# Performance work log

Measured on AMD Instinct MI355X. Metric: run time of the kernel, lower is better.

## Reference

```python
import jax, jax.numpy as jnp
import numpy as np


def setup_inputs() -> dict:
    key = jax.random.key(0)
    M, N = 2048, 16384
    x = jax.random.normal(key, (M, N), dtype=jnp.float32)
    # expk per DREAMPlace get_expk: exp(-j*pi*n/(2N)) stored as [N, 2] = (cos, -sin)
    ang = jnp.arange(N, dtype=jnp.float32) * np.float32(np.pi / (2.0 * N))
    expk = jnp.stack([jnp.cos(ang), -jnp.sin(ang)], axis=-1)
    return {"x": x, "expk": expk}


def reference(x, expk):
    """IDXCT: y_k = Re{ sum_{n=0}^{N-1} x_n * exp(j*pi/(2N) * n * (2k+1)) }.

    O(N log N) via the FFT trick:
      y_k = Re{ sum_n [x_n * exp(j*pi*n/(2N))] * exp(j*2*pi*n*k/(2N)) }
          = 2N * Re{ IFFT_{2N}(zero-padded v)[k] },  v_n = x_n * conj(expk_n)
    """
    N = x.shape[-1]
    # expk encodes exp(-j*pi*n/(2N)); we need its conjugate exp(+j*pi*n/(2N))
    v = x * (expk[..., 0] - 1j * expk[..., 1])  # complex64, [M, N]
    V = jnp.fft.ifft(v, n=2 * N, axis=-1)       # zero-padded to 2N
    y = (2 * N) * jnp.real(V[..., :N])
    return y.astype(x.dtype)
```

## Files before the change

### kernel.cpp

```cpp
#include <hip/hip_runtime.h>

#define PI_F 3.14159265358979323846f

constexpr int N_COLS   = 16384;
constexpr int HALF     = 8192;
constexpr int NTHREADS = 1024;

__device__ __forceinline__ int sw(int a) {
    return a ^ ((a >> 5) & 31) ^ ((a >> 10) & 31);
}

__global__ __launch_bounds__(NTHREADS)
void idxct_kernel(const float* __restrict__ x,
                  const float* __restrict__ expk,
                  float* __restrict__ y)
{
    __shared__ float sre[HALF];
    __shared__ float sim[HALF];

    const int row = blockIdx.x;
    const float* __restrict__ xr = x + (size_t)row * N_COLS;
    float* __restrict__ yr       = y + (size_t)row * N_COLS;
    const int t = threadIdx.x;
    const float x0 = xr[0];
    const float2* __restrict__ ek2 = (const float2*)expk;

    #pragma unroll
    for (int i = 0; i < HALF / NTHREADS; ++i) {
        int k = t + i * NTHREADS;
        float vkr, vki, c0, s0;
        {
            float2 e = ek2[k];
            c0 = e.x; s0 = -e.y;
            if (k == 0) { vkr = x0; vki = 0.0f; }
            else {
                float a = xr[k], b = xr[N_COLS - k];
                vkr = a * c0 + b * s0;
                vki = a * s0 - b * c0;
            }
        }
        float wkr, wki;
        {
            int K = k + HALF;
            float2 e = ek2[K];
            float c = e.x, s = -e.y;
            float a = xr[K], b = xr[N_COLS - K];
            wkr = a * c + b * s;
            wki = a * s - b * c;
        }
        float dr = vkr - wkr, di = vki - wki;
        float cA = c0 * c0 - s0 * s0, sA = 2.0f * c0 * s0;
        float ec = cA * cA - sA * sA, es = 2.0f * cA * sA;
        float zr = (vkr + wkr) - (ec * di + es * dr);
        float zi = (vki + wki) + (ec * dr - es * di);
        int rk = (int)(__brev((unsigned)k) >> 19);
        int pa = sw(rk);
        sre[pa] = zr;
        sim[pa] = zi;
    }

    __syncthreads();
    #pragma unroll
    for (int u = 0; u < 2; ++u) {
        int q = t + u * NTHREADS;
        int a0 = sw(q << 2);
        int a1 = a0 ^ 1, a2i = a0 ^ 2, a3 = a0 ^ 3;
        float r0 = sre[a0],  i0 = sim[a0];
        float r1 = sre[a1],  i1 = sim[a1];
        float r2 = sre[a2i], i2 = sim[a2i];
        float r3 = sre[a3],  i3 = sim[a3];
        float tr, ti;
        tr = r1;  ti = i1;  r1 = r0 - tr; i1 = i0 - ti; r0 += tr; i0 += ti;
        tr = r3;  ti = i3;  r3 = r2 - tr; i3 = i2 - ti; r2 += tr; i2 += ti;
        tr = r2;  ti = i2;  r2 = r0 - tr; i2 = i0 - ti; r0 += tr; i0 += ti;
        tr = -i3; ti = r3;  r3 = r1 - tr; i3 = i1 - ti; r1 += tr; i1 += ti;
        sre[a0]  = r0; sim[a0]  = i0;
        sre[a1]  = r1; sim[a1]  = i1;
        sre[a2i] = r2; sim[a2i] = i2;
        sre[a3]  = r3; sim[a3]  = i3;
    }

    #pragma unroll
    for (int p = 1; p < 6; ++p) {
        const int s = 1 << (2 * p);
        __syncthreads();
        #pragma unroll
        for (int u = 0; u < 2; ++u) {
            int q = t + u * NTHREADS;
            int j = q & (s - 1);
            int base = ((q >> (2 * p)) << (2 * p + 2)) + j;
            int a0 = sw(base);
            int a1 = sw(base + s);
            int a2i = sw(base + 2 * s);
            int a3 = sw(base + 3 * s);
            float r0 = sre[a0],  i0 = sim[a0];
            float r1 = sre[a1],  i1 = sim[a1];
            float r2 = sre[a2i], i2 = sim[a2i];
            float r3 = sre[a3],  i3 = sim[a3];
            float a2ang = (float)j * (PI_F / (float)(2 * s));
            float s2, c2; __sincosf(a2ang, &s2, &c2);
            float c1 = c2 * c2 - s2 * s2;
            float s1 = 2.0f * c2 * s2;
            float tr, ti;
            tr = c1 * r1 - s1 * i1; ti = c1 * i1 + s1 * r1;
            r1 = r0 - tr; i1 = i0 - ti; r0 += tr; i0 += ti;
            tr = c1 * r3 - s1 * i3; ti = c1 * i3 + s1 * r3;
            r3 = r2 - tr; i3 = i2 - ti; r2 += tr; i2 += ti;
            tr = c2 * r2 - s2 * i2; ti = c2 * i2 + s2 * r2;
            r2 = r0 - tr; i2 = i0 - ti; r0 += tr; i0 += ti;
            tr = -s2 * r3 - c2 * i3; ti = c2 * r3 - s2 * i3;
            r3 = r1 - tr; i3 = i1 - ti; r1 += tr; i1 += ti;
            sre[a0]  = r0; sim[a0]  = i0;
            sre[a1]  = r1; sim[a1]  = i1;
            sre[a2i] = r2; sim[a2i] = i2;
            sre[a3]  = r3; sim[a3]  = i3;
        }
    }

    __syncthreads();
    #pragma unroll
    for (int u = 0; u < 4; ++u) {
        int q = t + u * NTHREADS;
        float a = (float)q * (PI_F / 4096.0f);
        float sn, cs; __sincosf(a, &sn, &cs);
        int a0 = sw(q);
        int a1 = sw(q + 4096);
        float r0 = sre[a0], i0 = sim[a0];
        float r1 = sre[a1], i1 = sim[a1];
        float tr = cs * r1 - sn * i1;
        float ti = cs * i1 + sn * r1;
        sre[a0] = r0 + tr; sim[a0] = i0 + ti;
        sre[a1] = r0 - tr; sim[a1] = i0 - ti;
    }
    __syncthreads();

    #pragma unroll
    for (int i = 0; i < N_COLS / NTHREADS; ++i) {
        int q = t + i * NTHREADS;
        int pidx = (q & 1) ? (N_COLS - 1 - (q >> 1)) : (q >> 1);
        int zi = sw(pidx >> 1);
        float val = (pidx & 1) ? sim[zi] : sre[zi];
        yr[q] = 0.5f * (val + x0);
    }
}

extern "C" void kernel_launch(void* const* d_in, const int* in_sizes, int n_in,
                              void* d_out, int out_size, void* d_ws, size_t ws_size,
                              hipStream_t stream)
{
    const float* x    = (const float*)d_in[0];
    const float* expk = (const float*)d_in[1];
    float* y          = (float*)d_out;
    const int M = in_sizes[0] / N_COLS;
    idxct_kernel<<<dim3(M), dim3(NTHREADS), 0, stream>>>(x, expk, y);
}
```

Baseline: 259.9 us.

## Fuse final radix-2 stage into output pass and precompute per-thread twiddles

The last radix-2 FFT stage is merged into the output epilogue, which now reads the symmetric pairs m and N-1-m directly and writes float4 vectors to global memory. This removes one shared-memory round trip and a barrier. Twiddle factors for each radix-4 stage are computed once per thread before the FFT instead of calling sincos per butterfly. Bit-reversed swizzled addresses are built from per-thread constants with XOR offsets, and the launch bounds hint requests higher occupancy, which may add register pressure.

```diff
diff --git a/kernel.cpp b/kernel.cpp
--- a/kernel.cpp
+++ b/kernel.cpp
@@ -2,15 +2,18 @@
 
 #define PI_F 3.14159265358979323846f
 
-constexpr int N_COLS   = 16384;
-constexpr int HALF     = 8192;
-constexpr int NTHREADS = 1024;
+constexpr int N_COLS = 16384;
+constexpr int HALF   = 8192;
+constexpr int NT     = 1024;
 
-__device__ __forceinline__ int sw(int a) {
+__host__ __device__ constexpr int sw(int a) {
     return a ^ ((a >> 5) & 31) ^ ((a >> 10) & 31);
 }
+__host__ __device__ constexpr int br3(int c) {
+    return ((c & 1) << 2) | (c & 2) | ((c & 4) >> 2);
+}
 
-__global__ __launch_bounds__(NTHREADS)
+__global__ __launch_bounds__(NT, 8)
 void idxct_kernel(const float* __restrict__ x,
                   const float* __restrict__ expk,
                   float* __restrict__ y)
@@ -25,9 +28,10 @@
     const float x0 = xr[0];
     const float2* __restrict__ ek2 = (const float2*)expk;
 
+    const int spt = sw((int)(__brev((unsigned)t) >> 22) << 3);
     #pragma unroll
-    for (int i = 0; i < HALF / NTHREADS; ++i) {
-        int k = t + i * NTHREADS;
+    for (int i = 0; i < HALF / NT; ++i) {
+        int k = t + i * NT;
         float vkr, vki, c0, s0;
         {
             float2 e = ek2[k];
@@ -53,16 +57,26 @@
         float ec = cA * cA - sA * sA, es = 2.0f * cA * sA;
         float zr = (vkr + wkr) - (ec * di + es * dr);
         float zi = (vki + wki) + (ec * dr - es * di);
-        int rk = (int)(__brev((unsigned)k) >> 19);
-        int pa = sw(rk);
+        int pa = spt ^ br3(i);
         sre[pa] = zr;
         sim[pa] = zi;
+    }
+
+    float2 T[5], T6;
+    {
+        float sn, cs;
+        __sincosf((float)(t & 3)   * (PI_F / 8.0f),    &sn, &cs); T[0] = make_float2(cs, sn);
+        __sincosf((float)(t & 15)  * (PI_F / 32.0f),   &sn, &cs); T[1] = make_float2(cs, sn);
+        __sincosf((float)(t & 63)  * (PI_F / 128.0f),  &sn, &cs); T[2] = make_float2(cs, sn);
+        __sincosf((float)(t & 255) * (PI_F / 512.0f),  &sn, &cs); T[3] = make_float2(cs, sn);
+        __sincosf((float)t         * (PI_F / 2048.0f), &sn, &cs); T[4] = make_float2(cs, sn);
+        __sincosf((float)t         * (PI_F / 4096.0f), &sn, &cs); T6   = make_float2(cs, sn);
     }
 
     __syncthreads();
     #pragma unroll
     for (int u = 0; u < 2; ++u) {
-        int q = t + u * NTHREADS;
+        int q = t + u * NT;
         int a0 = sw(q << 2);
         int a1 = a0 ^ 1, a2i = a0 ^ 2, a3 = a0 ^ 3;
         float r0 = sre[a0],  i0 = sim[a0];
@@ -84,23 +98,22 @@
     for (int p = 1; p < 6; ++p) {
         const int s = 1 << (2 * p);
         __syncthreads();
+        const float c2 = T[p - 1].x, s2 = T[p - 1].y;
+        const float c1 = c2 * c2 - s2 * s2;
+        const float s1 = 2.0f * c2 * s2;
         #pragma unroll
         for (int u = 0; u < 2; ++u) {
-            int q = t + u * NTHREADS;
+            int q = t + u * NT;
             int j = q & (s - 1);
             int base = ((q >> (2 * p)) << (2 * p + 2)) + j;
-            int a0 = sw(base);
-            int a1 = sw(base + s);
-            int a2i = sw(base + 2 * s);
-            int a3 = sw(base + 3 * s);
+            int a0  = sw(base);
+            int a1  = a0 ^ sw(s);
+            int a2i = a0 ^ sw(2 * s);
+            int a3  = a0 ^ sw(3 * s);
             float r0 = sre[a0],  i0 = sim[a0];
             float r1 = sre[a1],  i1 = sim[a1];
             float r2 = sre[a2i], i2 = sim[a2i];
             float r3 = sre[a3],  i3 = sim[a3];
-            float a2ang = (float)j * (PI_F / (float)(2 * s));
-            float s2, c2; __sincosf(a2ang, &s2, &c2);
-            float c1 = c2 * c2 - s2 * s2;
-            float s1 = 2.0f * c2 * s2;
             float tr, ti;
             tr = c1 * r1 - s1 * i1; ti = c1 * i1 + s1 * r1;
             r1 = r0 - tr; i1 = i0 - ti; r0 += tr; i0 += ti;
@@ -116,31 +129,44 @@
             sre[a3]  = r3; sim[a3]  = i3;
         }
     }
-
-    __syncthreads();
-    #pragma unroll
-    for (int u = 0; u < 4; ++u) {
-        int q = t + u * NTHREADS;
-        float a = (float)q * (PI_F / 4096.0f);
-        float sn, cs; __sincosf(a, &sn, &cs);
-        int a0 = sw(q);
-        int a1 = sw(q + 4096);
-        float r0 = sre[a0], i0 = sim[a0];
-        float r1 = sre[a1], i1 = sim[a1];
-        float tr = cs * r1 - sn * i1;
-        float ti = cs * i1 + sn * r1;
-        sre[a0] = r0 + tr; sim[a0] = i0 + ti;
-        sre[a1] = r0 - tr; sim[a1] = i0 - ti;
-    }
     __syncthreads();
 
-    #pragma unroll
-    for (int i = 0; i < N_COLS / NTHREADS; ++i) {
-        int q = t + i * NTHREADS;
-        int pidx = (q & 1) ? (N_COLS - 1 - (q >> 1)) : (q >> 1);
-        int zi = sw(pidx >> 1);
-        float val = (pidx & 1) ? sim[zi] : sre[zi];
-        yr[q] = 0.5f * (val + x0);
+    {
+        const float2 C4 = make_float2(0.99999970586288222f,
+                                      7.6699031874270453e-4f);
+        constexpr float RT = 0.70710678118654752440f;
+        const int sct = sw(t);
+        const int scr = sct ^ sw(1023);
+        #pragma unroll
+        for (int i = 0; i < 4; ++i) {
+            const int m   = t + NT * i;
+            const int am  = sct ^ sw(NT * i);
+            const int ar  = scr ^ sw(NT * (3 - i));
+            const int am2 = am ^ sw(4096);
+            const int ar2 = ar ^ sw(4096);
+            float umr = sre[am],  umi = sim[am];
+            float vmr = sre[am2], vmi = sim[am2];
+            float urr = sre[ar],  uri = sim[ar];
+            float wrr = sre[ar2], wri = sim[ar2];
+            float exr, exi;
+            if      (i == 0) { exr = T6.x;                 exi = T6.y; }
+            else if (i == 1) { exr = (T6.x - T6.y) * RT;   exi = (T6.x + T6.y) * RT; }
+            else if (i == 2) { exr = -T6.y;                exi = T6.x; }
+            else             { exr = -(T6.x + T6.y) * RT;  exi = (T6.x - T6.y) * RT; }
+            float Fr = exr * C4.x - exi * C4.y;
+            float Fi = exr * C4.y + exi * C4.x;
+            float cwr = -Fr, swr = Fi;
+            float trm = exr * vmr - exi * vmi;
+            float tim = exr * vmi + exi * vmr;
+            float trr = cwr * wrr - swr * wri;
+            float tir = cwr * wri + swr * wrr;
+            float4 o;
+            o.x = 0.5f * ((umr + trm) + x0);
+            o.y = 0.5f * ((uri - tir) + x0);
+            o.z = 0.5f * ((umi + tim) + x0);
+            o.w = 0.5f * ((urr - trr) + x0);
+            *reinterpret_cast<float4*>(yr + 4 * m) = o;
+        }
     }
 }
 
@@ -152,5 +178,5 @@
     const float* expk = (const float*)d_in[1];
     float* y          = (float*)d_out;
     const int M = in_sizes[0] / N_COLS;
-    idxct_kernel<<<dim3(M), dim3(NTHREADS), 0, stream>>>(x, expk, y);
+    idxct_kernel<<<dim3(M), dim3(NT), 0, stream>>>(x, expk, y);
 }
```

Result: faster. 254.3 us (-2.2%).
